# Kernel tuning notes

Measured on AMD Instinct MI355X. Metric: run time of the kernel, lower is better.

## Reference

```python
import jax, jax.numpy as jnp
import numpy as np

N_NODES = 100000
N_EDGES = 1600000
N_RELS = 19
DIMS = [1, 128, 128, 64]  # in_degree feature -> dims


def setup_inputs() -> dict:
    key = jax.random.key(0)
    ks = jax.random.split(key, 12)
    src = jax.random.randint(ks[0], (N_EDGES,), 0, N_NODES, dtype=jnp.int64)
    dst = jax.random.randint(ks[1], (N_EDGES,), 0, N_NODES, dtype=jnp.int64)
    etypes = jax.random.randint(ks[2], (N_EDGES,), 0, N_RELS, dtype=jnp.int64)
    inp = {"src": src, "dst": dst, "etypes": etypes}
    for i, (din, dout) in enumerate(zip(DIMS[:-1], DIMS[1:])):
        s = 1.0 / np.sqrt(max(din, 1))
        inp[f"W{i}"] = jax.random.normal(ks[3 + 3 * i], (N_RELS, din, dout), jnp.float32) * s
        inp[f"Wloop{i}"] = jax.random.normal(ks[4 + 3 * i], (din, dout), jnp.float32) * s
        inp[f"b{i}"] = jnp.zeros((dout,), jnp.float32)
    inp["num_nodes"] = N_NODES
    return inp


def _rel_graph_conv(h, src, dst, etypes, W, Wloop, b, num_nodes, activation):
    # per-relation transform of every node: [N, R, dout]
    transformed = jnp.einsum('nd,rdo->nro', h, W)
    # gather message per edge by (src node, edge relation): [E, dout]
    msg = transformed[src, etypes]
    # scatter-sum to destination nodes
    agg = jax.ops.segment_sum(msg, dst, num_segments=num_nodes)
    out = agg + h @ Wloop + b
    if activation is not None:
        out = activation(out)
    return out


def reference(src, dst, etypes, W0, Wloop0, b0, W1, Wloop1, b1, W2, Wloop2, b2, num_nodes):
    # h = g.in_degrees().view(-1, 1).float()
    deg = jax.ops.segment_sum(jnp.ones_like(dst, dtype=jnp.float32), dst,
                              num_segments=num_nodes)
    h = deg[:, None]
    h = _rel_graph_conv(h, src, dst, etypes, W0, Wloop0, b0, num_nodes, jax.nn.relu)
    h = _rel_graph_conv(h, src, dst, etypes, W1, Wloop1, b1, num_nodes, jax.nn.relu)
    h = _rel_graph_conv(h, src, dst, etypes, W2, Wloop2, b2, num_nodes, None)
    return h
```

## Files before the change

### kernel.cpp

```cpp
#include <hip/hip_runtime.h>
#include <hip/hip_bf16.h>
#include <stdint.h>

#define N_NODES 100000
#define N_EDGES 1600000
#define N_RELS  19
#define NQ      4
#define QN      25000
#define QTILES  196
#define NBQ     98
#define NSB     (NQ * NBQ)
#define N_BUCK  (NQ * N_RELS)
#define NBIN    391
#define NGR     8
#define NBK8    (N_BUCK * NGR)
#define NBIN8   (NBIN * NGR)
#define NHC     (N_BUCK + NBIN)
#define NHC2    (2 * NHC)
#define MSGQ    460000
#define NCKQ    3700
#define NCK_TOT 14000
#define EPB     2048
#define S1B     782

typedef __attribute__((ext_vector_type(8))) short bf16x8;
typedef __attribute__((ext_vector_type(4))) float f32x4;
typedef __attribute__((ext_vector_type(4))) int   int4v;

__device__ __forceinline__ unsigned short f2bf(float x) {
  union { float f; unsigned u; } v; v.f = x;
  unsigned r = v.u + 0x7FFF + ((v.u >> 16) & 1);
  return (unsigned short)(r >> 16);
}
__device__ __forceinline__ float bf2f(unsigned short b) {
  union { unsigned u; float f; } v; v.u = ((unsigned)b) << 16; return v.f;
}

__global__ void k_prep_w(const float* W1, const float* W2,
                         const float* Wl1, const float* Wl2,
                         unsigned short* Wt1, unsigned short* Wt2,
                         unsigned short* Wtl1, unsigned short* Wtl2) {
  int i = blockIdx.x * 256 + threadIdx.x;
  const int s1 = N_RELS * 128 * 128;
  const int s2 = N_RELS * 64 * 128;
  const int s3 = 128 * 128;
  const int s4 = 64 * 128;
  if (i < s1) {
    int r = i / (128 * 128); int rem = i % (128 * 128);
    int n = rem / 128, k = rem % 128;
    Wt1[i] = f2bf(W1[((size_t)r * 128 + k) * 128 + n]);
  } else if (i < s1 + s2) {
    int j = i - s1;
    int r = j / (64 * 128); int rem = j % (64 * 128);
    int n = rem / 128, k = rem % 128;
    Wt2[j] = f2bf(W2[((size_t)r * 128 + k) * 64 + n]);
  } else if (i < s1 + s2 + s3) {
    int j = i - s1 - s2; int n = j / 128, k = j % 128;
    Wtl1[j] = f2bf(Wl1[k * 128 + n]);
  } else if (i < s1 + s2 + s3 + s4) {
    int j = i - s1 - s2 - s3; int n = j / 128, k = j % 128;
    Wtl2[j] = f2bf(Wl2[k * 64 + n]);
  }
}

__global__ void k_hist(const int* __restrict__ dst, const int* __restrict__ et,
                       int* __restrict__ bcount8, int* __restrict__ bincount8,
                       int* __restrict__ histAll) {
  __shared__ int hK[N_BUCK], hB[NBIN];
  __shared__ int sb[256];
  int t = threadIdx.x, g = blockIdx.x & (NGR - 1);
  for (int i = t; i < N_BUCK; i += 256) hK[i] = 0;
  for (int i = t; i < NBIN; i += 256) hB[i] = 0;
  __syncthreads();
  int e0 = blockIdx.x * EPB;
  for (int r = 0; r < EPB / 256; r++) {
    int e = e0 + r * 256 + t;
    if (e < N_EDGES) {
      int d = dst[e];
      atomicAdd(&hK[(d / QN) * N_RELS + et[e]], 1);
      atomicAdd(&hB[d >> 8], 1);
    }
  }
  __syncthreads();
  int* hout = histAll + (size_t)blockIdx.x * NHC2;
  for (int i = t; i < N_BUCK; i += 256) {
    hout[i] = hK[i];
    if (hK[i]) atomicAdd(&bcount8[i * NGR + g], hK[i]);
  }
  for (int i = t; i < NBIN; i += 256) {
    hout[N_BUCK + i] = hB[i];
    if (hB[i]) atomicAdd(&bincount8[i * NGR + g], hB[i]);
  }
  {
    int v0 = (2 * t < N_BUCK) ? hK[2 * t] : 0;
    int v1 = (2 * t + 1 < N_BUCK) ? hK[2 * t + 1] : 0;
    sb[t] = v0 + v1;
    __syncthreads();
    for (int s = 1; s < 256; s <<= 1) {
      int x = (t >= s) ? sb[t - s] : 0;
      __syncthreads();
      sb[t] += x;
      __syncthreads();
    }
    int base = sb[t] - v0 - v1;
    if (2 * t < N_BUCK) hout[NHC + 2 * t] = base;
    if (2 * t + 1 < N_BUCK) hout[NHC + 2 * t + 1] = base + v0;
    __syncthreads();
  }
  {
    int v0 = (2 * t < NBIN) ? hB[2 * t] : 0;
    int v1 = (2 * t + 1 < NBIN) ? hB[2 * t + 1] : 0;
    sb[t] = v0 + v1;
    __syncthreads();
    for (int s = 1; s < 256; s <<= 1) {
      int x = (t >= s) ? sb[t - s] : 0;
      __syncthreads();
      sb[t] += x;
      __syncthreads();
    }
    int base = sb[t] - v0 - v1;
    if (2 * t < NBIN) hout[NHC + N_BUCK + 2 * t] = base;
    if (2 * t + 1 < NBIN) hout[NHC + N_BUCK + 2 * t + 1] = base + v0;
  }
}

__global__ void k_scan0(const int* __restrict__ bcount8, const int* __restrict__ bincount8,
                        int* boff, int* bcur8, int* cbase, int* qcs, int* selfb,
                        int* binoff8, int* bincur8) {
  __shared__ int shK[NBK8];
  __shared__ int sb76[N_BUCK];
  __shared__ int sbs[N_BUCK];
  __shared__ int sh[512];
  int t = threadIdx.x;
  for (int i = t; i < NBK8; i += 512) shK[i] = bcount8[i];
  __syncthreads();
  if (t < N_BUCK) {
    int s = 0;
    for (int gg = 0; gg < NGR; gg++) s += shK[t * NGR + gg];
    sb76[t] = s;
  }
  __syncthreads();
  if (t == 0) {
    int a = 0, cb = 0;
    for (int q = 0; q < NQ; q++) {
      qcs[q] = cb;
      for (int r = 0; r < N_RELS; r++) {
        int b = q * N_RELS + r;
        boff[b] = a; sbs[b] = a; cbase[b] = cb;
        a += sb76[b]; cb += (sb76[b] + 127) >> 7;
      }
      selfb[q] = cb; cb += QTILES;
    }
    qcs[NQ] = cb;
    boff[N_BUCK] = a;
  }
  __syncthreads();
  for (int i = t; i < NBK8; i += 512) {
    int b = i >> 3, gg = i & (NGR - 1);
    int base = sbs[b];
    for (int k = 0; k < gg; k++) base += shK[b * NGR + k];
    bcur8[i] = base;
  }
  int vals[7];
  int i0 = t * 7;
  int loc = 0;
  for (int k = 0; k < 7; k++) {
    int i = i0 + k;
    int v = (i < NBIN8) ? bincount8[i] : 0;
    vals[k] = v; loc += v;
  }
  sh[t] = loc;
  __syncthreads();
  for (int s = 1; s < 512; s <<= 1) {
    int x = (t >= s) ? sh[t - s] : 0;
    __syncthreads();
    sh[t] += x;
    __syncthreads();
  }
  int run = sh[t] - loc;
  for (int k = 0; k < 7; k++) {
    int i = i0 + k;
    if (i < NBIN8) { binoff8[i] = run; bincur8[i] = run; run += vals[k]; }
  }
  if (t == 511) binoff8[NBIN8] = sh[511];
}

__launch_bounds__(256)
__global__ void k_scat1a(const int* __restrict__ src, const int* __restrict__ dst,
                         const int* __restrict__ et,
                         const int* __restrict__ histAll,
                         int* __restrict__ bcur8,
                         int* __restrict__ srcS, int* __restrict__ posE) {
  __shared__ int sortK[EPB];
  __shared__ int lK[N_BUCK], gKr[N_BUCK];
  int t = threadIdx.x, blk = blockIdx.x, g = blk & (NGR - 1);
  const int* hin = histAll + (size_t)blk * NHC2;
  for (int i = t; i < N_BUCK; i += 256) {
    int h = hin[i], l = hin[NHC + i];
    lK[i] = l;
    gKr[i] = h ? (atomicAdd(&bcur8[i * NGR + g], h) - l) : 0;
  }
  __syncthreads();
  int e0 = blk * EPB;
  int nval = min(EPB, N_EDGES - e0);
  for (int r = 0; r < EPB / 256; r++) {
    int e = e0 + r * 256 + t;
    if (e < N_EDGES) {
      int d = dst[e], rl = et[e], sv = src[e];
      int bk = (d / QN) * N_RELS + rl;
      int lrk = atomicAdd(&lK[bk], 1);
      sortK[lrk] = sv | (bk << 17);
      posE[e] = gKr[bk] + lrk;
    }
  }
  __syncthreads();
  for (int r = 0; r < EPB / 256; r++) {
    int s = r * 256 + t;
    if (s < nval) {
      int v = sortK[s];
      srcS[gKr[v >> 17] + s] = v & 0x1FFFF;
    }
  }
}

__launch_bounds__(256)
__global__ void k_scat1b(const int* __restrict__ src, const int* __restrict__ dst,
                         const int* __restrict__ et,
                         const int* __restrict__ posE,
                         const int* __restrict__ histAll,
                         int* __restrict__ bincur8,
                         int* __restrict__ stgA, int* __restrict__ stgB) {
  __shared__ int sortA[EPB], sortBv[EPB];
  __shared__ int lB[NBIN], gBr[NBIN];
  int t = threadIdx.x, blk = blockIdx.x, g = blk & (NGR - 1);
  const int* hin = histAll + (size_t)blk * NHC2;
  for (int i = t; i < NBIN; i += 256) {
    int h = hin[N_BUCK + i], l = hin[NHC + N_BUCK + i];
    lB[i] = l;
    gBr[i] = h ? (atomicAdd(&bincur8[i * NGR + g], h) - l) : 0;
  }
  __syncthreads();
  int e0 = blk * EPB;
  int nval = min(EPB, N_EDGES - e0);
  for (int r = 0; r < EPB / 256; r++) {
    int e = e0 + r * 256 + t;
    if (e < N_EDGES) {
      int d = dst[e], rl = et[e], sv = src[e];
      int gpos = posE[e];
      int bn = d >> 8;
      int lrb = atomicAdd(&lB[bn], 1);
      sortA[lrb] = gpos | (rl << 21) | ((bn & 63) << 26);
      sortBv[lrb] = sv | ((d & 255) << 17) | ((bn >> 6) << 25);
    }
  }
  __syncthreads();
  for (int r = 0; r < EPB / 256; r++) {
    int s = r * 256 + t;
    if (s < nval) {
      int a = sortA[s], b = sortBv[s];
      int bn = ((a >> 26) & 63) | (((b >> 25) & 7) << 6);
      int adr = gBr[bn] + s;
      stgA[adr] = a & 0x03FFFFFF;
      stgB[adr] = b & 0x01FFFFFF;
    }
  }
}

__global__ void k_cnt(const int* __restrict__ stgB, const int* __restrict__ binoff8,
                      int* __restrict__ ncount) {
  __shared__ int c[256];
  int b = blockIdx.x, t = threadIdx.x;
  c[t] = 0;
  __syncthreads();
  int lo = binoff8[b * NGR], hi = binoff8[b * NGR + NGR];
  for (int s = lo + t; s < hi; s += 256)
    atomicAdd(&c[(stgB[s] >> 17) & 255], 1);
  __syncthreads();
  int n = b * 256 + t;
  if (n < N_NODES) ncount[n] = c[t];
}

__global__ void k_scanA(const int* __restrict__ ncount, int* __restrict__ bsum) {
  __shared__ int sh[256];
  int b = blockIdx.x, t = threadIdx.x;
  int q = b / NBQ, bb = b % NBQ;
  int i = bb * 256 + t;
  int val = (i < QN) ? (ncount[q * QN + i] + 1) : 0;
  sh[t] = val;
  __syncthreads();
  for (int s = 128; s > 0; s >>= 1) {
    if (t < s) sh[t] += sh[t + s];
    __syncthreads();
  }
  if (t == 0) bsum[b] = sh[0];
}

__global__ void k_scanB(const int* bsum, int* bbase, int* nodeoff) {
  __shared__ int sh[NSB];
  int t = threadIdx.x;
  if (t < NSB) sh[t] = bsum[t];
  __syncthreads();
  if (t < NQ) {
    int a = 0;
    for (int i = 0; i < NBQ; i++) {
      int v = sh[t * NBQ + i]; sh[t * NBQ + i] = a; a += v;
    }
    nodeoff[(t + 1) * QN + t] = a;
  }
  __syncthreads();
  if (t < NSB) bbase[t] = sh[t];
}

__global__ void k_scanC(const int* __restrict__ ncount,
                        const int* __restrict__ bbase,
                        const int* __restrict__ boff,
                        int* __restrict__ nodeoff, int* __restrict__ ginv) {
  __shared__ int sh[256];
  int b = blockIdx.x, t = threadIdx.x;
  int q = b / NBQ, bb = b % NBQ;
  int i = bb * 256 + t;
  int val = (i < QN) ? (ncount[q * QN + i] + 1) : 0;
  sh[t] = val;
  __syncthreads();
  for (int s = 1; s < 256; s <<= 1) {
    int x = (t >= s) ? sh[t - s] : 0;
    __syncthreads();
    sh[t] += x;
    __syncthreads();
  }
  int excl = sh[t] - val + bbase[b];
  if (i < QN) {
    int n = q * QN + i;
    nodeoff[n + q] = excl;
    int qedges = boff[(q + 1) * N_RELS] - boff[q * N_RELS];
    ginv[(size_t)q * MSGQ + excl] = qedges + i;
  }
}

__global__ void k_scat2(const int* __restrict__ stgA, const int* __restrict__ stgB,
                        const int* __restrict__ binoff8,
                        const int* __restrict__ nodeoff,
                        const int* __restrict__ boff,
                        const int* __restrict__ ncount,
                        int* __restrict__ ginv, int* __restrict__ Rg) {
  __shared__ int cur[256];
  __shared__ int R[256][N_RELS];
  __shared__ int qe0s[NQ + 1];
  int b = blockIdx.x, t = threadIdx.x;
  if (t <= NQ) qe0s[t] = boff[t * N_RELS];
  int n = b * 256 + t;
  if (n < N_NODES) {
    int q = n / QN;
    cur[t] = nodeoff[n + q] + 1;
  }
#pragma unroll
  for (int r = 0; r < N_RELS; r++) R[t][r] = 0;
  __syncthreads();
  int lo = binoff8[b * NGR], hi = binoff8[b * NGR + NGR];
  for (int s = lo + t; s < hi; s += 256) {
    int a = stgA[s], bb = stgB[s];
    int dlow = (bb >> 17) & 255;
    int slot = atomicAdd(&cur[dlow], 1);
    int pos = a & 0x1FFFFF, rel = (a >> 21) & 31;
    int sv = bb & 0x1FFFF;
    int d = b * 256 + dlow;
    int q = d / QN;
    ginv[(size_t)q * MSGQ + slot] = pos - qe0s[q];
    atomicAdd(&R[dlow][rel], ncount[sv]);
  }
  __syncthreads();
  if (n < N_NODES) {
#pragma unroll
    for (int r = 0; r < N_RELS; r++)
      Rg[(size_t)r * N_NODES + n] = R[t][r];
  }
}

__launch_bounds__(256, 3)
__global__ void k_h1(const int* __restrict__ Rg, const int* __restrict__ ncount,
                     const float* __restrict__ W0, const float* __restrict__ Wl0,
                     const float* __restrict__ b0,
                     unsigned short* __restrict__ h1) {
  __shared__ float W0s[N_RELS * 128];
  __shared__ float wl[128], bb[128];
  __shared__ __align__(16) unsigned short Hs[128 * 128];
  int t = threadIdx.x, blk = blockIdx.x;
  for (int i = t; i < N_RELS * 128; i += 256) W0s[i] = W0[i];
  if (t < 128) { wl[t] = Wl0[t]; bb[t] = b0[t]; }
  __syncthreads();
  int n0 = blk * 128;
  int cnt = min(128, N_NODES - n0);
  int ln = t >> 1;
  int half = (t & 1) * 64;
  if (ln < cnt) {
    int n = n0 + ln;
    float rr[N_RELS];
#pragma unroll
    for (int r = 0; r < N_RELS; r++) rr[r] = (float)Rg[(size_t)r * N_NODES + n];
    float dn = (float)ncount[n];
    for (int c0 = half; c0 < half + 64; c0 += 8) {
      float acc[8];
#pragma unroll
      for (int j = 0; j < 8; j++) acc[j] = dn * wl[c0 + j] + bb[c0 + j];
      for (int r = 0; r < N_RELS; r++) {
#pragma unroll
        for (int j = 0; j < 8; j++)
          acc[j] += rr[r] * W0s[r * 128 + c0 + j];
      }
      unsigned vs[4];
#pragma unroll
      for (int j = 0; j < 4; j++) {
        float x0 = fmaxf(acc[2 * j], 0.f), x1 = fmaxf(acc[2 * j + 1], 0.f);
        vs[j] = (unsigned)f2bf(x0) | ((unsigned)f2bf(x1) << 16);
      }
      int4v o = {(int)vs[0], (int)vs[1], (int)vs[2], (int)vs[3]};
      *(int4v*)&Hs[ln * 128 + c0] = o;
    }
  }
  __syncthreads();
  int tot = cnt * 16;
  for (int task = t; task < tot; task += 256)
    *(int4v*)&h1[(size_t)n0 * 128 + task * 8] = *(const int4v*)&Hs[task * 8];
}

__global__ void k_fill(const int* boff, const int* cbase,
                       const int* selfb, int* cA, int* cB) {
  int b = blockIdx.x;
  if (b < N_BUCK) {
    int cnt = boff[b + 1] - boff[b], e0 = boff[b], w0 = cbase[b];
    int rel = b % N_RELS;
    int nch = (cnt + 127) >> 7;
    for (int i = threadIdx.x; i < nch; i += blockDim.x) {
      cA[w0 + i] = (e0 + i * 128) | (rel << 21);
      cB[w0 + i] = min(128, cnt - i * 128);
    }
  } else {
    int q = b - N_BUCK;
    int w0 = selfb[q];
    for (int i = threadIdx.x; i < QTILES; i += blockDim.x) {
      cA[w0 + i] = (i * 128) | (19 << 21);
      cB[w0 + i] = min(128, QN - i * 128);
    }
  }
}

template <int NOUT>
__launch_bounds__(256, NOUT == 64 ? 5 : 4)
__global__ void k_gemm_msg(const unsigned short* __restrict__ hprev,
                           const unsigned short* __restrict__ Wt,
                           const unsigned short* __restrict__ Wtl,
                           const int* __restrict__ qcs, int q,
                           const int* __restrict__ cA,
                           const int* __restrict__ cB,
                           const int* __restrict__ srcS,
                           const int* __restrict__ boff,
                           unsigned short* __restrict__ msg) {
  const int LDK = 136;
  const int CLD = NOUT + 8;
  const int SH = (NOUT * LDK > 128 * CLD) ? NOUT * LDK : 128 * CLD;
  __shared__ __align__(16) unsigned short Bs[SH];

  int cs = qcs[q], ce = qcs[q + 1];
  int w = blockIdx.x;
  if (w >= ce - cs) return;
  w += cs;
  int pa = cA[w];
  int e0 = pa & 0x1FFFFF, rel = pa >> 21;
  int cnt = cB[w];
  bool self = (rel == 19);
  const unsigned short* wsrc = self ? Wtl : (Wt + (size_t)rel * NOUT * 128);
  int qe0 = boff[q * N_RELS];
  int qedges = boff[(q + 1) * N_RELS] - qe0;
  int ppos0 = self ? (qedges + e0) : (e0 - qe0);
  int tid = threadIdx.x;
  const int lane = tid & 63, wid = tid >> 6;

  int rowg[2]; bool valv[2];
#pragma unroll
  for (int fi = 0; fi < 2; fi++) {
    int m = wid * 32 + fi * 16 + (lane & 15);
    bool v = m < cnt;
    valv[fi] = v;
    int row = 0;
    if (v) row = self ? (q * QN + e0 + m) : srcS[e0 + m];
    rowg[fi] = row;
  }
  bf16x8 a[2][4];
#pragma unroll
  for (int fi = 0; fi < 2; fi++) {
    const unsigned short* rp = hprev + (size_t)rowg[fi] * 128 + (lane >> 4) * 8;
#pragma unroll
    for (int kk = 0; kk < 4; kk++)
      a[fi][kk] = *(const bf16x8*)&rp[kk * 32];
  }
#pragma unroll
  for (int fi = 0; fi < 2; fi++)
    if (!valv[fi]) {
#pragma unroll
      for (int kk = 0; kk < 4; kk++)
        a[fi][kk] = (bf16x8){0, 0, 0, 0, 0, 0, 0, 0};
    }

  for (int task = tid; task < NOUT * 16; task += 256) {
    int n = task >> 4, c = task & 15;
    *(int4v*)&Bs[n * LDK + c * 8] = *(const int4v*)&wsrc[n * 128 + c * 8];
  }
  __syncthreads();

  const int FJ = NOUT / 16;
  f32x4 acc[2][FJ];
#pragma unroll
  for (int i = 0; i < 2; i++)
#pragma unroll
    for (int j = 0; j < FJ; j++) acc[i][j] = (f32x4){0.f, 0.f, 0.f, 0.f};

#pragma unroll
  for (int kk = 0; kk < 4; kk++) {
    int kof = kk * 32 + (lane >> 4) * 8;
    bf16x8 b[FJ];
#pragma unroll
    for (int fj = 0; fj < FJ; fj++)
      b[fj] = *(const bf16x8*)&Bs[(fj * 16 + (lane & 15)) * LDK + kof];
#pragma unroll
    for (int fi = 0; fi < 2; fi++)
#pragma unroll
      for (int fj = 0; fj < FJ; fj++)
        acc[fi][fj] = __builtin_amdgcn_mfma_f32_16x16x32_bf16(a[fi][kk], b[fj], acc[fi][fj], 0, 0, 0);
  }

  __syncthreads();
#pragma unroll
  for (int fi = 0; fi < 2; fi++)
#pragma unroll
    for (int fj = 0; fj < FJ; fj++)
#pragma unroll
      for (int j = 0; j < 4; j++) {
        int mrow = wid * 32 + fi * 16 + (lane >> 4) * 4 + j;
        int col = fj * 16 + (lane & 15);
        Bs[mrow * CLD + col] = f2bf(acc[fi][fj][j]);
      }
  __syncthreads();
  const int CW = NOUT / 8;
  for (int task = tid; task < cnt * CW; task += 256) {
    int row = task / CW, c = task % CW;
    *(int4v*)&msg[(size_t)(ppos0 + row) * NOUT + c * 8] =
        *(const int4v*)&Bs[row * CLD + c * 8];
  }
}

template <int NOUT>
__global__ void k_reduce(const unsigned short* __restrict__ msg,
                         const int* __restrict__ ginv,
                         const int* __restrict__ nodeoff, int q,
                         const float* __restrict__ bias, int do_relu,
                         unsigned short* __restrict__ outh,
                         float* __restrict__ outf) {
  int t = threadIdx.x;
  int rn = blockIdx.x * 8 + (t >> 5);
  if (rn >= QN) return;
  int n = q * QN + rn;
  int l = t & 31;
  int lo = nodeoff[n + q], hi = nodeoff[n + q + 1];
  const int* gv = ginv + (size_t)q * MSGQ;
  if (NOUT == 128) {
    float a0 = 0.f, a1 = 0.f, a2 = 0.f, a3 = 0.f;
    for (int i = lo; i < hi; i++) {
      int ppos = gv[i];
      uint2 v = *(const uint2*)&msg[(size_t)ppos * 128 + l * 4];
      a0 += bf2f((unsigned short)(v.x & 0xffff));
      a1 += bf2f((unsigned short)(v.x >> 16));
      a2 += bf2f((unsigned short)(v.y & 0xffff));
      a3 += bf2f((unsigned short)(v.y >> 16));
    }
    a0 += bias[l * 4];     a1 += bias[l * 4 + 1];
    a2 += bias[l * 4 + 2]; a3 += bias[l * 4 + 3];
    if (do_relu) {
      a0 = fmaxf(a0, 0.f); a1 = fmaxf(a1, 0.f);
      a2 = fmaxf(a2, 0.f); a3 = fmaxf(a3, 0.f);
    }
    uint2 o;
    o.x = (unsigned)f2bf(a0) | ((unsigned)f2bf(a1) << 16);
    o.y = (unsigned)f2bf(a2) | ((unsigned)f2bf(a3) << 16);
    *(uint2*)&outh[(size_t)n * 128 + l * 4] = o;
  } else {
    float a0 = 0.f, a1 = 0.f;
    for (int i = lo; i < hi; i++) {
      int ppos = gv[i];
      unsigned v = *(const unsigned*)&msg[(size_t)ppos * 64 + l * 2];
      a0 += bf2f((unsigned short)(v & 0xffff));
      a1 += bf2f((unsigned short)(v >> 16));
    }
    a0 += bias[l * 2];
    a1 += bias[l * 2 + 1];
    if (do_relu) { a0 = fmaxf(a0, 0.f); a1 = fmaxf(a1, 0.f); }
    outf[(size_t)n * 64 + l * 2]     = a0;
    outf[(size_t)n * 64 + l * 2 + 1] = a1;
  }
}

extern "C" void kernel_launch(void* const* d_in, const int* in_sizes, int n_in,
                              void* d_out, int out_size, void* d_ws, size_t ws_size,
                              hipStream_t stream) {
  const int* src = (const int*)d_in[0];
  const int* dst = (const int*)d_in[1];
  const int* et  = (const int*)d_in[2];
  const float* W0  = (const float*)d_in[3];
  const float* Wl0 = (const float*)d_in[4];
  const float* b0  = (const float*)d_in[5];
  const float* W1  = (const float*)d_in[6];
  const float* Wl1 = (const float*)d_in[7];
  const float* b1  = (const float*)d_in[8];
  const float* W2  = (const float*)d_in[9];
  const float* Wl2 = (const float*)d_in[10];
  const float* b2  = (const float*)d_in[11];

  char* ws = (char*)d_ws;
  size_t off = 0;
  auto alloc = [&](size_t bytes) {
    void* p = ws + off;
    off = (off + bytes + 255) & ~(size_t)255;
    return p;
  };
  unsigned short* msg = (unsigned short*)alloc((size_t)MSGQ * 128 * 2);
  unsigned short* h1 = (unsigned short*)alloc((size_t)N_NODES * 128 * 2);
  unsigned short* h2 = (unsigned short*)alloc((size_t)N_NODES * 128 * 2);
  int* srcS = (int*)alloc((size_t)N_EDGES * 4);
  int* stgA = (int*)alloc((size_t)N_EDGES * 4);
  int* stgB = (int*)alloc((size_t)N_EDGES * 4);
  int* posE = (int*)alloc((size_t)N_EDGES * 4);
  int* ginv = (int*)alloc((size_t)NQ * MSGQ * 4);
  int* Rg   = (int*)alloc((size_t)N_RELS * N_NODES * 4);
  int* ncount  = (int*)alloc((size_t)N_NODES * 4);
  int* nodeoff = (int*)alloc((size_t)(N_NODES + NQ + 4) * 4);
  int* histAll = (int*)alloc((size_t)S1B * NHC2 * 4);
  unsigned short* Wt1  = (unsigned short*)alloc((size_t)N_RELS * 128 * 128 * 2);
  unsigned short* Wt2  = (unsigned short*)alloc((size_t)N_RELS * 64 * 128 * 2);
  unsigned short* Wtl1 = (unsigned short*)alloc((size_t)128 * 128 * 2);
  unsigned short* Wtl2 = (unsigned short*)alloc((size_t)64 * 128 * 2);
  int* acc0 = (int*)alloc((size_t)(NBK8 + NBIN8) * 4);
  int* bcount8   = acc0;
  int* bincount8 = acc0 + NBK8;
  int* ints = (int*)alloc(4096);
  int* boff   = ints;
  int* cbase  = ints + 80;
  int* qcs    = ints + 160;
  int* selfb  = ints + 168;
  int* bcur8  = (int*)alloc((size_t)NBK8 * 4);
  int* binoff8 = (int*)alloc((size_t)(NBIN8 + 1) * 4);
  int* bincur8 = (int*)alloc((size_t)NBIN8 * 4);
  int* bsum  = (int*)alloc((size_t)NSB * 4);
  int* bbase = (int*)alloc((size_t)NSB * 4);
  int* cA = (int*)alloc((size_t)NCK_TOT * 4);
  int* cB = (int*)alloc((size_t)NCK_TOT * 4);

  hipMemsetAsync(acc0, 0, (size_t)(NBK8 + NBIN8) * 4, stream);

  k_prep_w<<<1920, 256, 0, stream>>>(W1, W2, Wl1, Wl2, Wt1, Wt2, Wtl1, Wtl2);
  k_hist<<<S1B, 256, 0, stream>>>(dst, et, bcount8, bincount8, histAll);
  k_scan0<<<1, 512, 0, stream>>>(bcount8, bincount8, boff, bcur8, cbase, qcs,
                                 selfb, binoff8, bincur8);
  k_scat1a<<<S1B, 256, 0, stream>>>(src, dst, et, histAll, bcur8, srcS, posE);
  k_scat1b<<<S1B, 256, 0, stream>>>(src, dst, et, posE, histAll, bincur8,
                                    stgA, stgB);
  k_cnt<<<NBIN, 256, 0, stream>>>(stgB, binoff8, ncount);
  k_scanA<<<NSB, 256, 0, stream>>>(ncount, bsum);
  k_scanB<<<1, 512, 0, stream>>>(bsum, bbase, nodeoff);
  k_scanC<<<NSB, 256, 0, stream>>>(ncount, bbase, boff, nodeoff, ginv);
  k_scat2<<<NBIN, 256, 0, stream>>>(stgA, stgB, binoff8, nodeoff, boff,
                                    ncount, ginv, Rg);
  k_fill<<<N_BUCK + NQ, 256, 0, stream>>>(boff, cbase, selfb, cA, cB);
  k_h1<<<(N_NODES + 127) / 128, 256, 0, stream>>>(Rg, ncount, W0, Wl0, b0, h1);

  for (int q = 0; q < NQ; q++) {
    k_gemm_msg<128><<<NCKQ, 256, 0, stream>>>(h1, Wt1, Wtl1, qcs, q, cA, cB,
                                              srcS, boff, msg);
    k_reduce<128><<<QN / 8, 256, 0, stream>>>(msg, ginv, nodeoff, q, b1, 1,
                                              h2, nullptr);
  }
  for (int q = 0; q < NQ; q++) {
    k_gemm_msg<64><<<NCKQ, 256, 0, stream>>>(h2, Wt2, Wtl2, qcs, q, cA, cB,
                                             srcS, boff, msg);
    k_reduce<64><<<QN / 8, 256, 0, stream>>>(msg, ginv, nodeoff, q, b2, 0,
                                             nullptr, (float*)d_out);
  }
}
```

Before: 719.1 us.

## Scatter GEMM messages directly into destination-sorted order, drop gather index in reduce

The inverse permutation (slot to message position) becomes a forward map (message position to destination slot). The message GEMM now writes each output row straight to its destination-sorted slot, so the reduce kernel reads contiguous rows without an index lookup. This removes a dependent index load and random row gathers in the reduce, but the GEMM epilogue now does scattered 16-byte row writes plus one index load per row.

```diff
diff --git a/kernel.cpp b/kernel.cpp
--- a/kernel.cpp
+++ b/kernel.cpp
@@ -314,7 +314,7 @@
 __global__ void k_scanC(const int* __restrict__ ncount,
                         const int* __restrict__ bbase,
                         const int* __restrict__ boff,
-                        int* __restrict__ nodeoff, int* __restrict__ ginv) {
+                        int* __restrict__ nodeoff, int* __restrict__ gfwd) {
   __shared__ int sh[256];
   int b = blockIdx.x, t = threadIdx.x;
   int q = b / NBQ, bb = b % NBQ;
@@ -333,7 +333,7 @@
     int n = q * QN + i;
     nodeoff[n + q] = excl;
     int qedges = boff[(q + 1) * N_RELS] - boff[q * N_RELS];
-    ginv[(size_t)q * MSGQ + excl] = qedges + i;
+    gfwd[(size_t)q * MSGQ + qedges + i] = excl;
   }
 }
 
@@ -342,7 +342,7 @@
                         const int* __restrict__ nodeoff,
                         const int* __restrict__ boff,
                         const int* __restrict__ ncount,
-                        int* __restrict__ ginv, int* __restrict__ Rg) {
+                        int* __restrict__ gfwd, int* __restrict__ Rg) {
   __shared__ int cur[256];
   __shared__ int R[256][N_RELS];
   __shared__ int qe0s[NQ + 1];
@@ -365,7 +365,7 @@
     int sv = bb & 0x1FFFF;
     int d = b * 256 + dlow;
     int q = d / QN;
-    ginv[(size_t)q * MSGQ + slot] = pos - qe0s[q];
+    gfwd[(size_t)q * MSGQ + (pos - qe0s[q])] = slot;
     atomicAdd(&R[dlow][rel], ncount[sv]);
   }
   __syncthreads();
@@ -454,6 +454,7 @@
                            const int* __restrict__ cB,
                            const int* __restrict__ srcS,
                            const int* __restrict__ boff,
+                           const int* __restrict__ gfwd,
                            unsigned short* __restrict__ msg) {
   const int LDK = 136;
   const int CLD = NOUT + 8;
@@ -543,14 +544,14 @@
   const int CW = NOUT / 8;
   for (int task = tid; task < cnt * CW; task += 256) {
     int row = task / CW, c = task % CW;
-    *(int4v*)&msg[(size_t)(ppos0 + row) * NOUT + c * 8] =
+    int slot = gfwd[ppos0 + row];
+    *(int4v*)&msg[(size_t)slot * NOUT + c * 8] =
         *(const int4v*)&Bs[row * CLD + c * 8];
   }
 }
 
 template <int NOUT>
 __global__ void k_reduce(const unsigned short* __restrict__ msg,
-                         const int* __restrict__ ginv,
                          const int* __restrict__ nodeoff, int q,
                          const float* __restrict__ bias, int do_relu,
                          unsigned short* __restrict__ outh,
@@ -561,12 +562,10 @@
   int n = q * QN + rn;
   int l = t & 31;
   int lo = nodeoff[n + q], hi = nodeoff[n + q + 1];
-  const int* gv = ginv + (size_t)q * MSGQ;
   if (NOUT == 128) {
     float a0 = 0.f, a1 = 0.f, a2 = 0.f, a3 = 0.f;
     for (int i = lo; i < hi; i++) {
-      int ppos = gv[i];
-      uint2 v = *(const uint2*)&msg[(size_t)ppos * 128 + l * 4];
+      uint2 v = *(const uint2*)&msg[(size_t)i * 128 + l * 4];
       a0 += bf2f((unsigned short)(v.x & 0xffff));
       a1 += bf2f((unsigned short)(v.x >> 16));
       a2 += bf2f((unsigned short)(v.y & 0xffff));
@@ -585,8 +584,7 @@
   } else {
     float a0 = 0.f, a1 = 0.f;
     for (int i = lo; i < hi; i++) {
-      int ppos = gv[i];
-      unsigned v = *(const unsigned*)&msg[(size_t)ppos * 64 + l * 2];
+      unsigned v = *(const unsigned*)&msg[(size_t)i * 64 + l * 2];
       a0 += bf2f((unsigned short)(v & 0xffff));
       a1 += bf2f((unsigned short)(v >> 16));
     }
@@ -628,7 +626,7 @@
   int* stgA = (int*)alloc((size_t)N_EDGES * 4);
   int* stgB = (int*)alloc((size_t)N_EDGES * 4);
   int* posE = (int*)alloc((size_t)N_EDGES * 4);
-  int* ginv = (int*)alloc((size_t)NQ * MSGQ * 4);
+  int* gfwd = (int*)alloc((size_t)NQ * MSGQ * 4);
   int* Rg   = (int*)alloc((size_t)N_RELS * N_NODES * 4);
   int* ncount  = (int*)alloc((size_t)N_NODES * 4);
   int* nodeoff = (int*)alloc((size_t)(N_NODES + NQ + 4) * 4);
@@ -665,22 +663,24 @@
   k_cnt<<<NBIN, 256, 0, stream>>>(stgB, binoff8, ncount);
   k_scanA<<<NSB, 256, 0, stream>>>(ncount, bsum);
   k_scanB<<<1, 512, 0, stream>>>(bsum, bbase, nodeoff);
-  k_scanC<<<NSB, 256, 0, stream>>>(ncount, bbase, boff, nodeoff, ginv);
+  k_scanC<<<NSB, 256, 0, stream>>>(ncount, bbase, boff, nodeoff, gfwd);
   k_scat2<<<NBIN, 256, 0, stream>>>(stgA, stgB, binoff8, nodeoff, boff,
-                                    ncount, ginv, Rg);
+                                    ncount, gfwd, Rg);
   k_fill<<<N_BUCK + NQ, 256, 0, stream>>>(boff, cbase, selfb, cA, cB);
   k_h1<<<(N_NODES + 127) / 128, 256, 0, stream>>>(Rg, ncount, W0, Wl0, b0, h1);
 
   for (int q = 0; q < NQ; q++) {
     k_gemm_msg<128><<<NCKQ, 256, 0, stream>>>(h1, Wt1, Wtl1, qcs, q, cA, cB,
-                                              srcS, boff, msg);
-    k_reduce<128><<<QN / 8, 256, 0, stream>>>(msg, ginv, nodeoff, q, b1, 1,
+                                              srcS, boff,
+                                              gfwd + (size_t)q * MSGQ, msg);
+    k_reduce<128><<<QN / 8, 256, 0, stream>>>(msg, nodeoff, q, b1, 1,
                                               h2, nullptr);
   }
   for (int q = 0; q < NQ; q++) {
     k_gemm_msg<64><<<NCKQ, 256, 0, stream>>>(h2, Wt2, Wtl2, qcs, q, cA, cB,
-                                             srcS, boff, msg);
-    k_reduce<64><<<QN / 8, 256, 0, stream>>>(msg, ginv, nodeoff, q, b2, 0,
+                                             srcS, boff,
+                                             gfwd + (size_t)q * MSGQ, msg);
+    k_reduce<64><<<QN / 8, 256, 0, stream>>>(msg, nodeoff, q, b2, 0,
                                              nullptr, (float*)d_out);
   }
 }
```

Result: faster. 658.4 us (-8.4%).
